# Optimization experiments

Measured on AMD Instinct MI355X. Metric: run time of the kernel, lower is better.

## Reference

```python
import jax, jax.numpy as jnp
import numpy as np

N_BOX = 1000000


def box2corners(box):
    # box: (N,5) = x,y,w,h,alpha -> corners (N,4,2), order matches lilanxiao/Rotated_IoU
    x, y, w, h, a = (box[:, i] for i in range(5))
    dx = jnp.array([0.5, -0.5, -0.5, 0.5], box.dtype)
    dy = jnp.array([0.5, 0.5, -0.5, -0.5], box.dtype)
    cx = dx[None, :] * w[:, None]
    cy = dy[None, :] * h[:, None]
    c, s = jnp.cos(a)[:, None], jnp.sin(a)[:, None]
    rx = cx * c - cy * s + x[:, None]
    ry = cx * s + cy * c + y[:, None]
    return jnp.stack([rx, ry], axis=-1)


def edge_intersections(c1, c2):
    # all 4x4 edge-pair intersections; strict interior criterion (0<t<1, 0<u<1)
    p1, p2 = c1, jnp.roll(c1, -1, axis=1)
    p3, p4 = c2, jnp.roll(c2, -1, axis=1)
    x1, y1 = p1[:, :, None, 0], p1[:, :, None, 1]
    x2, y2 = p2[:, :, None, 0], p2[:, :, None, 1]
    x3, y3 = p3[:, None, :, 0], p3[:, None, :, 1]
    x4, y4 = p4[:, None, :, 0], p4[:, None, :, 1]
    num_t = (x2 - x1) * (y3 - y1) - (y2 - y1) * (x3 - x1)
    den_t = (x2 - x1) * (y3 - y4) - (y2 - y1) * (x3 - x4)
    t = jnp.where(den_t == 0., -1., num_t / jnp.where(den_t == 0., 1., den_t))
    mask_t = (t > 0.) & (t < 1.)
    num_u = (x4 - x3) * (y1 - y3) - (y4 - y3) * (x1 - x3)
    den_u = (x4 - x3) * (y1 - y2) - (y4 - y3) * (x1 - x2)
    u = jnp.where(den_u == 0., -1., num_u / jnp.where(den_u == 0., 1., den_u))
    mask = mask_t & (u > 0.) & (u < 1.)
    tx = x1 + t * (x2 - x1)
    ty = y1 + t * (y2 - y1)
    pts = jnp.stack([tx, ty], axis=-1) * mask[..., None]
    n = c1.shape[0]
    return pts.reshape(n, 16, 2), mask.reshape(n, 16)


def box_in_box(corners1, corners2):
    # projection test: is each corner of box1 inside rectangle box2
    a = corners2[:, 0:1, :]
    b = corners2[:, 1:2, :]
    d = corners2[:, 3:4, :]
    ab, ad, am = b - a, d - a, corners1 - a
    p_ab = (ab * am).sum(-1) / (ab * ab).sum(-1)
    p_ad = (ad * am).sum(-1) / (ad * ad).sum(-1)
    eps = 1e-6
    return (p_ab > -eps) & (p_ab < 1. + eps) & (p_ad > -eps) & (p_ad < 1. + eps)


def intersection_area(c1, c2):
    # convex intersection polygon: 24 candidate vertices, sort valid ones by angle, shoelace
    pts, m_int = edge_intersections(c1, c2)
    m1 = box_in_box(c1, c2)
    m2 = box_in_box(c2, c1)
    verts = jnp.concatenate([c1, c2, pts], axis=1)   # (N,24,2)
    mask = jnp.concatenate([m1, m2, m_int], axis=1)  # (N,24)
    k = mask.sum(axis=1)
    mean = (verts * mask[..., None]).sum(1, keepdims=True) / jnp.maximum(k, 1)[:, None, None]
    v = jnp.where(mask[..., None], verts - mean, 0.)
    ang = jnp.where(mask, jnp.arctan2(v[..., 1], v[..., 0]), 1e9)
    order = jnp.argsort(ang, axis=1)
    vs = jnp.take_along_axis(v, order[..., None], axis=1)
    pad = jnp.arange(24)[None, :, None] < k[:, None, None]
    vs = jnp.where(pad, vs, vs[:, 0:1, :])  # pad by repeating first valid vertex -> zero cross terms
    vn = jnp.roll(vs, -1, axis=1)
    cross = vs[..., 0] * vn[..., 1] - vs[..., 1] * vn[..., 0]
    return 0.5 * jnp.abs(cross.sum(axis=1))


def riou_loss(pred, target):
    # RIOUloss(reduction='none', loss_type='iou') -> cal_diou per-box loss, loss[0]
    rad_p = jnp.arctan2(pred[:, 4], pred[:, 5])
    rad_t = jnp.arctan2(target[:, 4], target[:, 5])
    b1 = jnp.concatenate([pred[:, :4], rad_p[:, None]], axis=1)
    b2 = jnp.concatenate([target[:, :4], rad_t[:, None]], axis=1)
    c1 = box2corners(b1)
    c2 = box2corners(b2)
    inter = intersection_area(c1, c2)
    area1 = b1[:, 2] * b1[:, 3]
    area2 = b2[:, 2] * b2[:, 3]
    union = area1 + area2 - inter
    iou = inter / union
    allc = jnp.concatenate([c1, c2], axis=1)  # (N,8,2) enclosing box (axis-aligned)
    wc = allc[..., 0].max(1) - allc[..., 0].min(1)
    hc = allc[..., 1].max(1) - allc[..., 1].min(1)
    c2diag = wc * wc + hc * hc
    d2 = (b1[:, 0] - b2[:, 0]) ** 2 + (b1[:, 1] - b2[:, 1]) ** 2
    return 1. - iou + d2 / c2diag


def setup_inputs() -> dict:
    key = jax.random.key(0)
    k1, k2, k3, k4 = jax.random.split(key, 4)
    n = N_BOX
    xy = jax.random.uniform(k1, (n, 2)) * 640.
    wh = jax.random.uniform(k2, (n, 2)) * 48. + 2.
    sc = jax.random.normal(k3, (n, 2)) + 0.1
    pred = jnp.concatenate([xy, wh, sc], axis=1)
    k5, k6, k7 = jax.random.split(k4, 3)
    t_xy = xy + jax.random.normal(k5, (n, 2)) * 8.
    t_wh = jnp.abs(wh * (1. + 0.2 * jax.random.normal(k6, (n, 2)))) + 1.
    t_sc = sc + 0.3 * jax.random.normal(k7, (n, 2))
    target = jnp.concatenate([t_xy, t_wh, t_sc], axis=1)
    return {"pred": pred, "target": target}


def reference(pred, target):
    return riou_loss(pred, target)
```

## Files before the change

kernel.cpp:

```cpp
#include <hip/hip_runtime.h>
#include <math.h>


#define FMUL __fmul_rn
#define FADD __fadd_rn
#define FSUB __fsub_rn
#define FDIV __fdiv_rn

__device__ __forceinline__ float rcpf_(float x) { return __builtin_amdgcn_rcpf(x); }

#define CE(A,B) do { unsigned _x = pk[A], _y = pk[B]; \
                     pk[A] = _x < _y ? _x : _y; pk[B] = _x < _y ? _y : _x; } while (0)

#define SORT8(o) do { \
    CE(o+0,o+1); CE(o+2,o+3); CE(o+0,o+2); CE(o+1,o+3); CE(o+1,o+2); \
    CE(o+4,o+5); CE(o+6,o+7); CE(o+4,o+6); CE(o+5,o+7); CE(o+5,o+6); \
    CE(o+0,o+4); CE(o+1,o+5); CE(o+2,o+6); CE(o+3,o+7); \
    CE(o+2,o+4); CE(o+3,o+5); \
    CE(o+1,o+2); CE(o+3,o+4); CE(o+5,o+6); } while (0)

#define MERGE_LOW8(o) do { \
    CE(0,o+7); CE(1,o+6); CE(2,o+5); CE(3,o+4); \
    CE(4,o+3); CE(5,o+2); CE(6,o+1); CE(7,o+0); \
    CE(0,4); CE(1,5); CE(2,6); CE(3,7); \
    CE(0,2); CE(1,3); CE(4,6); CE(5,7); \
    CE(0,1); CE(2,3); CE(4,5); CE(6,7); } while (0)

#define MAKEKEY(J, WX, WY, M, DST) do {                                     \
    float _dsum = FADD(fabsf(WX), fabsf(WY));                               \
    float _rs = (_dsum > 0.0f) ? FMUL((WX), rcpf_(_dsum)) : 1.0f;           \
    float _keyf = copysignf(FSUB(1.0f, _rs), (WY));                         \
    unsigned _sbk = __float_as_uint(_keyf);                                 \
    unsigned _u = _sbk ^ (unsigned)(((int)_sbk >> 31) | (int)0x80000000);   \
    (DST) = (M) ? ((_u & 0xFFFFFFE0u) | (unsigned)(J))                      \
                : (0xFFFFFFE0u | (unsigned)(J));                            \
} while (0)

__global__
__attribute__((amdgpu_flat_work_group_size(256, 256), amdgpu_waves_per_eu(1)))
void riou_kernel(const float* __restrict__ pred,
                 const float* __restrict__ tgt,
                 float* __restrict__ out, int n)
{
    __shared__ float2 vlds[24][256];
    const int tid = threadIdx.x;
    int i = blockIdx.x * blockDim.x + tid;
    if (i >= n) return;

    const float2* p2 = (const float2*)(pred + 6 * (size_t)i);
    const float2* q2 = (const float2*)(tgt  + 6 * (size_t)i);
    float2 pa = p2[0], pb = p2[1], pc2 = p2[2];
    float2 qa = q2[0], qb = q2[1], qc2 = q2[2];
    const float px = pa.x, py = pa.y, pw = pb.x, ph = pb.y;
    const float qx = qa.x, qy = qa.y, qw = qb.x, qh = qb.y;

    float rad1 = atan2f(pc2.x, pc2.y);
    float cA = cosf(rad1), sA = sinf(rad1);
    float rad2 = atan2f(qc2.x, qc2.y);
    float cB = cosf(rad2), sB = sinf(rad2);

    const float ddx[4] = {0.5f, -0.5f, -0.5f, 0.5f};
    const float ddy[4] = {0.5f, 0.5f, -0.5f, -0.5f};
    float c1x[4], c1y[4], c2x[4], c2y[4];
#pragma unroll
    for (int j = 0; j < 4; j++) {
        float cx = FMUL(ddx[j], pw), cy = FMUL(ddy[j], ph);
        c1x[j] = FADD(FSUB(FMUL(cx, cA), FMUL(cy, sA)), px);
        c1y[j] = FADD(FADD(FMUL(cx, sA), FMUL(cy, cA)), py);
        float dx2 = FMUL(ddx[j], qw), dy2 = FMUL(ddy[j], qh);
        c2x[j] = FADD(FSUB(FMUL(dx2, cB), FMUL(dy2, sB)), qx);
        c2y[j] = FADD(FADD(FMUL(dx2, sB), FMUL(dy2, cB)), qy);
        vlds[j][tid]     = make_float2(c1x[j], c1y[j]);
        vlds[4 + j][tid] = make_float2(c2x[j], c2y[j]);
    }

    float minx = c1x[0], maxx = c1x[0], miny = c1y[0], maxy = c1y[0];
#pragma unroll
    for (int j = 1; j < 4; j++) {
        minx = fminf(minx, c1x[j]); maxx = fmaxf(maxx, c1x[j]);
        miny = fminf(miny, c1y[j]); maxy = fmaxf(maxy, c1y[j]);
    }
#pragma unroll
    for (int j = 0; j < 4; j++) {
        minx = fminf(minx, c2x[j]); maxx = fmaxf(maxx, c2x[j]);
        miny = fminf(miny, c2y[j]); maxy = fmaxf(maxy, c2y[j]);
    }
    float wcb = FSUB(maxx, minx), hcb = FSUB(maxy, miny);
    float c2d = FADD(FMUL(wcb, wcb), FMUL(hcb, hcb));
    float dxc = FSUB(px, qx), dyc = FSUB(py, qy);
    float d2 = FADD(FMUL(dxc, dxc), FMUL(dyc, dyc));

    unsigned mbits = 0;
    float sx = 0.0f, sy = 0.0f;
    const float eps = 1e-6f;
    const float hieps = 1.0f + 1e-6f;

    {
        float ax = c2x[0], ay = c2y[0];
        float abx = FSUB(c2x[1], ax), aby = FSUB(c2y[1], ay);
        float adx = FSUB(c2x[3], ax), ady = FSUB(c2y[3], ay);
        float rab = rcpf_(FADD(FMUL(abx, abx), FMUL(aby, aby)));
        float rad = rcpf_(FADD(FMUL(adx, adx), FMUL(ady, ady)));
#pragma unroll
        for (int j = 0; j < 4; j++) {
            float amx = FSUB(c1x[j], ax), amy = FSUB(c1y[j], ay);
            float pab = FMUL(FADD(FMUL(abx, amx), FMUL(aby, amy)), rab);
            float pad = FMUL(FADD(FMUL(adx, amx), FMUL(ady, amy)), rad);
            int m = (pab > -eps) & (pab < hieps) & (pad > -eps) & (pad < hieps);
            mbits |= (unsigned)m << j;
            sx = FADD(sx, m ? c1x[j] : 0.0f);
            sy = FADD(sy, m ? c1y[j] : 0.0f);
        }
    }
    {
        float ax = c1x[0], ay = c1y[0];
        float abx = FSUB(c1x[1], ax), aby = FSUB(c1y[1], ay);
        float adx = FSUB(c1x[3], ax), ady = FSUB(c1y[3], ay);
        float rab = rcpf_(FADD(FMUL(abx, abx), FMUL(aby, aby)));
        float rad = rcpf_(FADD(FMUL(adx, adx), FMUL(ady, ady)));
#pragma unroll
        for (int j = 0; j < 4; j++) {
            float amx = FSUB(c2x[j], ax), amy = FSUB(c2y[j], ay);
            float pab = FMUL(FADD(FMUL(abx, amx), FMUL(aby, amy)), rab);
            float pad = FMUL(FADD(FMUL(adx, amx), FMUL(ady, amy)), rad);
            int m = (pab > -eps) & (pab < hieps) & (pad > -eps) & (pad < hieps);
            mbits |= (unsigned)m << (4 + j);
            sx = FADD(sx, m ? c2x[j] : 0.0f);
            sy = FADD(sy, m ? c2y[j] : 0.0f);
        }
    }
    float fex[4], fey[4];
#pragma unroll
    for (int e2 = 0; e2 < 4; e2++) {
        fex[e2] = FSUB(c2x[(e2 + 1) & 3], c2x[e2]);
        fey[e2] = FSUB(c2y[(e2 + 1) & 3], c2y[e2]);
    }
#pragma unroll
    for (int e1 = 0; e1 < 4; e1++) {
        float x1 = c1x[e1], y1 = c1y[e1];
        float ex = FSUB(c1x[(e1 + 1) & 3], x1), ey = FSUB(c1y[(e1 + 1) & 3], y1);
#pragma unroll
        for (int e2 = 0; e2 < 4; e2++) {
            float dx31 = FSUB(c2x[e2], x1), dy31 = FSUB(c2y[e2], y1);
            float num_t = FSUB(FMUL(ex, dy31), FMUL(ey, dx31));
            float den_t = FSUB(FMUL(ey, fex[e2]), FMUL(ex, fey[e2]));
            float rd = rcpf_(den_t);
            float tq = FMUL(num_t, rd);
            float num_u = FSUB(FMUL(fey[e2], dx31), FMUL(fex[e2], dy31));
            float uq = FMUL(num_u, rd);
            int m = (tq > 0.0f) & (tq < 1.0f) & (uq < 0.0f) & (uq > -1.0f);
            float ix = FADD(x1, FMUL(tq, ex));
            float iy = FADD(y1, FMUL(tq, ey));
            int s = 4 * e1 + e2;
            vlds[8 + s][tid] = make_float2(ix, iy);
            mbits |= (unsigned)m << (8 + s);
            sx = FADD(sx, m ? ix : 0.0f);
            sy = FADD(sy, m ? iy : 0.0f);
        }
    }

    int k = __popc(mbits);

    float kk = (float)(k > 0 ? k : 1);
    float mx = FDIV(sx, kk), my = FDIV(sy, kk);

    unsigned pk[24];
    float2 va[8];
#pragma unroll
    for (int j = 0; j < 8; j++) va[j] = vlds[8 + j][tid];
#pragma unroll
    for (int j = 0; j < 8; j++) {
        float rx = (j < 4) ? c1x[j] : c2x[j - 4];
        float ry = (j < 4) ? c1y[j] : c2y[j - 4];
        int m = (mbits >> j) & 1u;
        float wx2 = FSUB(rx, mx);
        float wy2 = FSUB(ry, my);
        MAKEKEY(j, wx2, wy2, m, pk[j]);
    }
#pragma unroll
    for (int j = 8; j < 16; j++) {
        int m = (mbits >> j) & 1u;
        float wx2 = FSUB(va[j - 8].x, mx);
        float wy2 = FSUB(va[j - 8].y, my);
        MAKEKEY(j, wx2, wy2, m, pk[j]);
    }
#pragma unroll
    for (int j = 0; j < 8; j++) va[j] = vlds[16 + j][tid];
#pragma unroll
    for (int j = 16; j < 24; j++) {
        int m = (mbits >> j) & 1u;
        float wx2 = FSUB(va[j - 16].x, mx);
        float wy2 = FSUB(va[j - 16].y, my);
        MAKEKEY(j, wx2, wy2, m, pk[j]);
    }

    SORT8(0);
    SORT8(8);
    SORT8(16);
    MERGE_LOW8(8);
    MERGE_LOW8(16);

    float2 vi[8];
#pragma unroll
    for (int s = 0; s < 8; s++) {
        unsigned row = pk[s] & 31u;
        vi[s] = vlds[row][tid];
    }

    float firstx = 0.0f, firsty = 0.0f, prevx = 0.0f, prevy = 0.0f;
    float crs = 0.0f;
#pragma unroll
    for (int s = 0; s < 8; s++) {
        float gx = FSUB(vi[s].x, mx);
        float gy = FSUB(vi[s].y, my);
        bool act = s < k;
        float bx = act ? gx : prevx;
        float by = act ? gy : prevy;
        if (s == 0) { firstx = bx; firsty = by; }
        else {
            crs = FADD(crs, FSUB(FMUL(prevx, by), FMUL(prevy, bx)));
        }
        prevx = bx; prevy = by;
    }
    if (k > 8) {
        for (int s = 8; s < k; s++) {
            unsigned mn = pk[8];
#pragma unroll
            for (int j = 9; j < 24; j++) mn = (pk[j] < mn) ? pk[j] : mn;
            float2 vt = vlds[mn & 31u][tid];
            float bx = FSUB(vt.x, mx);
            float by = FSUB(vt.y, my);
            crs = FADD(crs, FSUB(FMUL(prevx, by), FMUL(prevy, bx)));
            prevx = bx; prevy = by;
#pragma unroll
            for (int j = 8; j < 24; j++) if (pk[j] == mn) pk[j] = 0xFFFFFFFFu;
        }
    }
    crs = FADD(crs, FSUB(FMUL(prevx, firsty), FMUL(prevy, firstx)));
    float inter = FMUL(0.5f, fabsf(crs));

    float area1 = FMUL(pw, ph), area2 = FMUL(qw, qh);
    float uni = FSUB(FADD(area1, area2), inter);
    float iou = FMUL(inter, rcpf_(uni));

    out[i] = FADD(FSUB(1.0f, iou), FMUL(d2, rcpf_(c2d)));
}

extern "C" void kernel_launch(void* const* d_in, const int* in_sizes, int n_in,
                              void* d_out, int out_size, void* d_ws, size_t ws_size,
                              hipStream_t stream) {
    const float* pred = (const float*)d_in[0];
    const float* tgt  = (const float*)d_in[1];
    float* out = (float*)d_out;
    int n = in_sizes[0] / 6;
    int block = 256;
    int grid = (n + block - 1) / block;
    riou_kernel<<<grid, block, 0, stream>>>(pred, tgt, out, n);
}
```

Measured before the change: 110.5 us.

## Vectorize geometry with packed float2 math and split LDS into SoA rows

```diff
diff --git a/kernel.cpp b/kernel.cpp
--- a/kernel.cpp
+++ b/kernel.cpp
@@ -7,6 +7,9 @@
 #define FSUB __fsub_rn
 #define FDIV __fdiv_rn
 
+typedef float v2f __attribute__((ext_vector_type(2)));
+__device__ __forceinline__ v2f v2(float a, float b) { v2f r; r.x = a; r.y = b; return r; }
+__device__ __forceinline__ v2f vs(float a) { return v2(a, a); }
 __device__ __forceinline__ float rcpf_(float x) { return __builtin_amdgcn_rcpf(x); }
 
 #define CE(A,B) do { unsigned _x = pk[A], _y = pk[B]; \
@@ -36,13 +39,16 @@
                 : (0xFFFFFFE0u | (unsigned)(J));                            \
 } while (0)
 
+#define LN(P, J) (((J) & 1) ? P[(J) >> 1].y : P[(J) >> 1].x)
+
 __global__
 __attribute__((amdgpu_flat_work_group_size(256, 256), amdgpu_waves_per_eu(1)))
 void riou_kernel(const float* __restrict__ pred,
                  const float* __restrict__ tgt,
                  float* __restrict__ out, int n)
 {
-    __shared__ float2 vlds[24][256];
+    __shared__ __align__(16) float ldsX[256][26];
+    __shared__ __align__(16) float ldsY[256][26];
     const int tid = threadIdx.x;
     int i = blockIdx.x * blockDim.x + tid;
     if (i >= n) return;
@@ -54,36 +60,47 @@
     const float px = pa.x, py = pa.y, pw = pb.x, ph = pb.y;
     const float qx = qa.x, qy = qa.y, qw = qb.x, qh = qb.y;
 
+    float area1 = FMUL(pw, ph), area2 = FMUL(qw, qh);
+
     float rad1 = atan2f(pc2.x, pc2.y);
     float cA = cosf(rad1), sA = sinf(rad1);
     float rad2 = atan2f(qc2.x, qc2.y);
     float cB = cosf(rad2), sB = sinf(rad2);
 
-    const float ddx[4] = {0.5f, -0.5f, -0.5f, 0.5f};
-    const float ddy[4] = {0.5f, 0.5f, -0.5f, -0.5f};
-    float c1x[4], c1y[4], c2x[4], c2y[4];
+    v2f c1xp[2], c1yp[2], c2xp[2], c2yp[2];
+    {
+        const v2f dx01 = v2(0.5f, -0.5f), dx23 = v2(-0.5f, 0.5f);
+        const v2f dy01 = v2(0.5f, 0.5f),  dy23 = v2(-0.5f, -0.5f);
+        v2f cxx01 = dx01 * vs(pw), cxx23 = dx23 * vs(pw);
+        v2f cyy01 = dy01 * vs(ph), cyy23 = dy23 * vs(ph);
+        c1xp[0] = (cxx01 * vs(cA) - cyy01 * vs(sA)) + vs(px);
+        c1xp[1] = (cxx23 * vs(cA) - cyy23 * vs(sA)) + vs(px);
+        c1yp[0] = (cxx01 * vs(sA) + cyy01 * vs(cA)) + vs(py);
+        c1yp[1] = (cxx23 * vs(sA) + cyy23 * vs(cA)) + vs(py);
+        v2f qxx01 = dx01 * vs(qw), qxx23 = dx23 * vs(qw);
+        v2f qyy01 = dy01 * vs(qh), qyy23 = dy23 * vs(qh);
+        c2xp[0] = (qxx01 * vs(cB) - qyy01 * vs(sB)) + vs(qx);
+        c2xp[1] = (qxx23 * vs(cB) - qyy23 * vs(sB)) + vs(qx);
+        c2yp[0] = (qxx01 * vs(sB) + qyy01 * vs(cB)) + vs(qy);
+        c2yp[1] = (qxx23 * vs(sB) + qyy23 * vs(cB)) + vs(qy);
+    }
+    *(v2f*)&ldsX[tid][0] = c1xp[0]; *(v2f*)&ldsX[tid][2] = c1xp[1];
+    *(v2f*)&ldsX[tid][4] = c2xp[0]; *(v2f*)&ldsX[tid][6] = c2xp[1];
+    *(v2f*)&ldsY[tid][0] = c1yp[0]; *(v2f*)&ldsY[tid][2] = c1yp[1];
+    *(v2f*)&ldsY[tid][4] = c2yp[0]; *(v2f*)&ldsY[tid][6] = c2yp[1];
+
+    float minx = c1xp[0].x, maxx = c1xp[0].x;
+    float miny = c1yp[0].x, maxy = c1yp[0].x;
+    minx = fminf(minx, c1xp[0].y); maxx = fmaxf(maxx, c1xp[0].y);
+    miny = fminf(miny, c1yp[0].y); maxy = fmaxf(maxy, c1yp[0].y);
+    minx = fminf(minx, c1xp[1].x); maxx = fmaxf(maxx, c1xp[1].x);
+    miny = fminf(miny, c1yp[1].x); maxy = fmaxf(maxy, c1yp[1].x);
+    minx = fminf(minx, c1xp[1].y); maxx = fmaxf(maxx, c1xp[1].y);
+    miny = fminf(miny, c1yp[1].y); maxy = fmaxf(maxy, c1yp[1].y);
 #pragma unroll
     for (int j = 0; j < 4; j++) {
-        float cx = FMUL(ddx[j], pw), cy = FMUL(ddy[j], ph);
-        c1x[j] = FADD(FSUB(FMUL(cx, cA), FMUL(cy, sA)), px);
-        c1y[j] = FADD(FADD(FMUL(cx, sA), FMUL(cy, cA)), py);
-        float dx2 = FMUL(ddx[j], qw), dy2 = FMUL(ddy[j], qh);
-        c2x[j] = FADD(FSUB(FMUL(dx2, cB), FMUL(dy2, sB)), qx);
-        c2y[j] = FADD(FADD(FMUL(dx2, sB), FMUL(dy2, cB)), qy);
-        vlds[j][tid]     = make_float2(c1x[j], c1y[j]);
-        vlds[4 + j][tid] = make_float2(c2x[j], c2y[j]);
-    }
-
-    float minx = c1x[0], maxx = c1x[0], miny = c1y[0], maxy = c1y[0];
-#pragma unroll
-    for (int j = 1; j < 4; j++) {
-        minx = fminf(minx, c1x[j]); maxx = fmaxf(maxx, c1x[j]);
-        miny = fminf(miny, c1y[j]); maxy = fmaxf(maxy, c1y[j]);
-    }
-#pragma unroll
-    for (int j = 0; j < 4; j++) {
-        minx = fminf(minx, c2x[j]); maxx = fmaxf(maxx, c2x[j]);
-        miny = fminf(miny, c2y[j]); maxy = fmaxf(maxy, c2y[j]);
+        minx = fminf(minx, LN(c2xp, j)); maxx = fmaxf(maxx, LN(c2xp, j));
+        miny = fminf(miny, LN(c2yp, j)); maxy = fmaxf(maxy, LN(c2yp, j));
     }
     float wcb = FSUB(maxx, minx), hcb = FSUB(maxy, miny);
     float c2d = FADD(FMUL(wcb, wcb), FMUL(hcb, hcb));
@@ -91,128 +108,187 @@
     float d2 = FADD(FMUL(dxc, dxc), FMUL(dyc, dyc));
 
     unsigned mbits = 0;
-    float sx = 0.0f, sy = 0.0f;
+    v2f s2 = v2(0.0f, 0.0f);
+    const v2f zero2 = v2(0.0f, 0.0f);
     const float eps = 1e-6f;
     const float hieps = 1.0f + 1e-6f;
 
     {
-        float ax = c2x[0], ay = c2y[0];
-        float abx = FSUB(c2x[1], ax), aby = FSUB(c2y[1], ay);
-        float adx = FSUB(c2x[3], ax), ady = FSUB(c2y[3], ay);
+        float ax = c2xp[0].x, ay = c2yp[0].x;
+        float abx = FSUB(c2xp[0].y, ax), aby = FSUB(c2yp[0].y, ay);
+        float adx = FSUB(c2xp[1].y, ax), ady = FSUB(c2yp[1].y, ay);
         float rab = rcpf_(FADD(FMUL(abx, abx), FMUL(aby, aby)));
         float rad = rcpf_(FADD(FMUL(adx, adx), FMUL(ady, ady)));
+        v2f amx01 = c1xp[0] - vs(ax), amx23 = c1xp[1] - vs(ax);
+        v2f amy01 = c1yp[0] - vs(ay), amy23 = c1yp[1] - vs(ay);
+        v2f pab01 = (vs(abx) * amx01 + vs(aby) * amy01) * vs(rab);
+        v2f pab23 = (vs(abx) * amx23 + vs(aby) * amy23) * vs(rab);
+        v2f pad01 = (vs(adx) * amx01 + vs(ady) * amy01) * vs(rad);
+        v2f pad23 = (vs(adx) * amx23 + vs(ady) * amy23) * vs(rad);
 #pragma unroll
         for (int j = 0; j < 4; j++) {
-            float amx = FSUB(c1x[j], ax), amy = FSUB(c1y[j], ay);
-            float pab = FMUL(FADD(FMUL(abx, amx), FMUL(aby, amy)), rab);
-            float pad = FMUL(FADD(FMUL(adx, amx), FMUL(ady, amy)), rad);
+            float pab = (j < 2) ? ((j & 1) ? pab01.y : pab01.x)
+                                : ((j & 1) ? pab23.y : pab23.x);
+            float pad = (j < 2) ? ((j & 1) ? pad01.y : pad01.x)
+                                : ((j & 1) ? pad23.y : pad23.x);
             int m = (pab > -eps) & (pab < hieps) & (pad > -eps) & (pad < hieps);
             mbits |= (unsigned)m << j;
-            sx = FADD(sx, m ? c1x[j] : 0.0f);
-            sy = FADD(sy, m ? c1y[j] : 0.0f);
-        }
-    }
-    {
-        float ax = c1x[0], ay = c1y[0];
-        float abx = FSUB(c1x[1], ax), aby = FSUB(c1y[1], ay);
-        float adx = FSUB(c1x[3], ax), ady = FSUB(c1y[3], ay);
+            s2 = s2 + (m ? v2(LN(c1xp, j), LN(c1yp, j)) : zero2);
+        }
+    }
+    {
+        float ax = c1xp[0].x, ay = c1yp[0].x;
+        float abx = FSUB(c1xp[0].y, ax), aby = FSUB(c1yp[0].y, ay);
+        float adx = FSUB(c1xp[1].y, ax), ady = FSUB(c1yp[1].y, ay);
         float rab = rcpf_(FADD(FMUL(abx, abx), FMUL(aby, aby)));
         float rad = rcpf_(FADD(FMUL(adx, adx), FMUL(ady, ady)));
+        v2f amx01 = c2xp[0] - vs(ax), amx23 = c2xp[1] - vs(ax);
+        v2f amy01 = c2yp[0] - vs(ay), amy23 = c2yp[1] - vs(ay);
+        v2f pab01 = (vs(abx) * amx01 + vs(aby) * amy01) * vs(rab);
+        v2f pab23 = (vs(abx) * amx23 + vs(aby) * amy23) * vs(rab);
+        v2f pad01 = (vs(adx) * amx01 + vs(ady) * amy01) * vs(rad);
+        v2f pad23 = (vs(adx) * amx23 + vs(ady) * amy23) * vs(rad);
 #pragma unroll
         for (int j = 0; j < 4; j++) {
-            float amx = FSUB(c2x[j], ax), amy = FSUB(c2y[j], ay);
-            float pab = FMUL(FADD(FMUL(abx, amx), FMUL(aby, amy)), rab);
-            float pad = FMUL(FADD(FMUL(adx, amx), FMUL(ady, amy)), rad);
+            float pab = (j < 2) ? ((j & 1) ? pab01.y : pab01.x)
+                                : ((j & 1) ? pab23.y : pab23.x);
+            float pad = (j < 2) ? ((j & 1) ? pad01.y : pad01.x)
+                                : ((j & 1) ? pad23.y : pad23.x);
             int m = (pab > -eps) & (pab < hieps) & (pad > -eps) & (pad < hieps);
             mbits |= (unsigned)m << (4 + j);
-            sx = FADD(sx, m ? c2x[j] : 0.0f);
-            sy = FADD(sy, m ? c2y[j] : 0.0f);
-        }
-    }
-    float fex[4], fey[4];
-#pragma unroll
-    for (int e2 = 0; e2 < 4; e2++) {
-        fex[e2] = FSUB(c2x[(e2 + 1) & 3], c2x[e2]);
-        fey[e2] = FSUB(c2y[(e2 + 1) & 3], c2y[e2]);
-    }
+            s2 = s2 + (m ? v2(LN(c2xp, j), LN(c2yp, j)) : zero2);
+        }
+    }
+    v2f fexx01, fexx23, feyy01, feyy23;
+    fexx01.x = FSUB(c2xp[0].y, c2xp[0].x);
+    fexx01.y = FSUB(c2xp[1].x, c2xp[0].y);
+    fexx23.x = FSUB(c2xp[1].y, c2xp[1].x);
+    fexx23.y = FSUB(c2xp[0].x, c2xp[1].y);
+    feyy01.x = FSUB(c2yp[0].y, c2yp[0].x);
+    feyy01.y = FSUB(c2yp[1].x, c2yp[0].y);
+    feyy23.x = FSUB(c2yp[1].y, c2yp[1].x);
+    feyy23.y = FSUB(c2yp[0].x, c2yp[1].y);
 #pragma unroll
     for (int e1 = 0; e1 < 4; e1++) {
-        float x1 = c1x[e1], y1 = c1y[e1];
-        float ex = FSUB(c1x[(e1 + 1) & 3], x1), ey = FSUB(c1y[(e1 + 1) & 3], y1);
+        float x1 = LN(c1xp, e1), y1 = LN(c1yp, e1);
+        float xn = LN(c1xp, (e1 + 1) & 3), yn = LN(c1yp, (e1 + 1) & 3);
+        float ex = FSUB(xn, x1), ey = FSUB(yn, y1);
+        v2f d31x01 = c2xp[0] - vs(x1), d31x23 = c2xp[1] - vs(x1);
+        v2f d31y01 = c2yp[0] - vs(y1), d31y23 = c2yp[1] - vs(y1);
+        v2f numt01 = vs(ex) * d31y01 - vs(ey) * d31x01;
+        v2f numt23 = vs(ex) * d31y23 - vs(ey) * d31x23;
+        v2f dent01 = vs(ey) * fexx01 - vs(ex) * feyy01;
+        v2f dent23 = vs(ey) * fexx23 - vs(ex) * feyy23;
+        v2f rd01, rd23;
+        rd01.x = rcpf_(dent01.x); rd01.y = rcpf_(dent01.y);
+        rd23.x = rcpf_(dent23.x); rd23.y = rcpf_(dent23.y);
+        v2f tq01 = numt01 * rd01, tq23 = numt23 * rd23;
+        v2f numu01 = feyy01 * d31x01 - fexx01 * d31y01;
+        v2f numu23 = feyy23 * d31x23 - fexx23 * d31y23;
+        v2f uq01 = numu01 * rd01, uq23 = numu23 * rd23;
+        v2f ixx01 = vs(x1) + tq01 * vs(ex), ixx23 = vs(x1) + tq23 * vs(ex);
+        v2f iyy01 = vs(y1) + tq01 * vs(ey), iyy23 = vs(y1) + tq23 * vs(ey);
+        int cb = 8 + 4 * e1;
+        *(v2f*)&ldsX[tid][cb]     = ixx01;
+        *(v2f*)&ldsX[tid][cb + 2] = ixx23;
+        *(v2f*)&ldsY[tid][cb]     = iyy01;
+        *(v2f*)&ldsY[tid][cb + 2] = iyy23;
 #pragma unroll
         for (int e2 = 0; e2 < 4; e2++) {
-            float dx31 = FSUB(c2x[e2], x1), dy31 = FSUB(c2y[e2], y1);
-            float num_t = FSUB(FMUL(ex, dy31), FMUL(ey, dx31));
-            float den_t = FSUB(FMUL(ey, fex[e2]), FMUL(ex, fey[e2]));
-            float rd = rcpf_(den_t);
-            float tq = FMUL(num_t, rd);
-            float num_u = FSUB(FMUL(fey[e2], dx31), FMUL(fex[e2], dy31));
-            float uq = FMUL(num_u, rd);
+            float tq = (e2 < 2) ? ((e2 & 1) ? tq01.y : tq01.x)
+                                : ((e2 & 1) ? tq23.y : tq23.x);
+            float uq = (e2 < 2) ? ((e2 & 1) ? uq01.y : uq01.x)
+                                : ((e2 & 1) ? uq23.y : uq23.x);
+            float ixv = (e2 < 2) ? ((e2 & 1) ? ixx01.y : ixx01.x)
+                                 : ((e2 & 1) ? ixx23.y : ixx23.x);
+            float iyv = (e2 < 2) ? ((e2 & 1) ? iyy01.y : iyy01.x)
+                                 : ((e2 & 1) ? iyy23.y : iyy23.x);
             int m = (tq > 0.0f) & (tq < 1.0f) & (uq < 0.0f) & (uq > -1.0f);
-            float ix = FADD(x1, FMUL(tq, ex));
-            float iy = FADD(y1, FMUL(tq, ey));
-            int s = 4 * e1 + e2;
-            vlds[8 + s][tid] = make_float2(ix, iy);
-            mbits |= (unsigned)m << (8 + s);
-            sx = FADD(sx, m ? ix : 0.0f);
-            sy = FADD(sy, m ? iy : 0.0f);
+            mbits |= (unsigned)m << (cb + e2);
+            s2 = s2 + (m ? v2(ixv, iyv) : zero2);
         }
     }
 
     int k = __popc(mbits);
 
     float kk = (float)(k > 0 ? k : 1);
-    float mx = FDIV(sx, kk), my = FDIV(sy, kk);
+    float mx = FDIV(s2.x, kk), my = FDIV(s2.y, kk);
 
     unsigned pk[24];
-    float2 va[8];
-#pragma unroll
-    for (int j = 0; j < 8; j++) va[j] = vlds[8 + j][tid];
-#pragma unroll
-    for (int j = 0; j < 8; j++) {
-        float rx = (j < 4) ? c1x[j] : c2x[j - 4];
-        float ry = (j < 4) ? c1y[j] : c2y[j - 4];
-        int m = (mbits >> j) & 1u;
-        float wx2 = FSUB(rx, mx);
-        float wy2 = FSUB(ry, my);
-        MAKEKEY(j, wx2, wy2, m, pk[j]);
-    }
-#pragma unroll
-    for (int j = 8; j < 16; j++) {
-        int m = (mbits >> j) & 1u;
-        float wx2 = FSUB(va[j - 8].x, mx);
-        float wy2 = FSUB(va[j - 8].y, my);
-        MAKEKEY(j, wx2, wy2, m, pk[j]);
-    }
-#pragma unroll
-    for (int j = 0; j < 8; j++) va[j] = vlds[16 + j][tid];
-#pragma unroll
-    for (int j = 16; j < 24; j++) {
-        int m = (mbits >> j) & 1u;
-        float wx2 = FSUB(va[j - 16].x, mx);
-        float wy2 = FSUB(va[j - 16].y, my);
-        MAKEKEY(j, wx2, wy2, m, pk[j]);
-    }
-
+    v2f bx0 = *(v2f*)&ldsX[tid][8],  bx1 = *(v2f*)&ldsX[tid][10];
+    v2f bx2 = *(v2f*)&ldsX[tid][12], bx3 = *(v2f*)&ldsX[tid][14];
+    v2f by0 = *(v2f*)&ldsY[tid][8],  by1 = *(v2f*)&ldsY[tid][10];
+    v2f by2 = *(v2f*)&ldsY[tid][12], by3 = *(v2f*)&ldsY[tid][14];
+    {
+        v2f wx, wy;
+        wx = c1xp[0] - vs(mx); wy = c1yp[0] - vs(my);
+        MAKEKEY(0, wx.x, wy.x, (int)((mbits >> 0) & 1u), pk[0]);
+        MAKEKEY(1, wx.y, wy.y, (int)((mbits >> 1) & 1u), pk[1]);
+        wx = c1xp[1] - vs(mx); wy = c1yp[1] - vs(my);
+        MAKEKEY(2, wx.x, wy.x, (int)((mbits >> 2) & 1u), pk[2]);
+        MAKEKEY(3, wx.y, wy.y, (int)((mbits >> 3) & 1u), pk[3]);
+        wx = c2xp[0] - vs(mx); wy = c2yp[0] - vs(my);
+        MAKEKEY(4, wx.x, wy.x, (int)((mbits >> 4) & 1u), pk[4]);
+        MAKEKEY(5, wx.y, wy.y, (int)((mbits >> 5) & 1u), pk[5]);
+        wx = c2xp[1] - vs(mx); wy = c2yp[1] - vs(my);
+        MAKEKEY(6, wx.x, wy.x, (int)((mbits >> 6) & 1u), pk[6]);
+        MAKEKEY(7, wx.y, wy.y, (int)((mbits >> 7) & 1u), pk[7]);
+    }
     SORT8(0);
+    {
+        v2f wx, wy;
+        wx = bx0 - vs(mx); wy = by0 - vs(my);
+        MAKEKEY(8, wx.x, wy.x, (int)((mbits >> 8) & 1u), pk[8]);
+        MAKEKEY(9, wx.y, wy.y, (int)((mbits >> 9) & 1u), pk[9]);
+        wx = bx1 - vs(mx); wy = by1 - vs(my);
+        MAKEKEY(10, wx.x, wy.x, (int)((mbits >> 10) & 1u), pk[10]);
+        MAKEKEY(11, wx.y, wy.y, (int)((mbits >> 11) & 1u), pk[11]);
+        wx = bx2 - vs(mx); wy = by2 - vs(my);
+        MAKEKEY(12, wx.x, wy.x, (int)((mbits >> 12) & 1u), pk[12]);
+        MAKEKEY(13, wx.y, wy.y, (int)((mbits >> 13) & 1u), pk[13]);
+        wx = bx3 - vs(mx); wy = by3 - vs(my);
+        MAKEKEY(14, wx.x, wy.x, (int)((mbits >> 14) & 1u), pk[14]);
+        MAKEKEY(15, wx.y, wy.y, (int)((mbits >> 15) & 1u), pk[15]);
+    }
+    bx0 = *(v2f*)&ldsX[tid][16]; bx1 = *(v2f*)&ldsX[tid][18];
+    bx2 = *(v2f*)&ldsX[tid][20]; bx3 = *(v2f*)&ldsX[tid][22];
+    by0 = *(v2f*)&ldsY[tid][16]; by1 = *(v2f*)&ldsY[tid][18];
+    by2 = *(v2f*)&ldsY[tid][20]; by3 = *(v2f*)&ldsY[tid][22];
     SORT8(8);
+    {
+        v2f wx, wy;
+        wx = bx0 - vs(mx); wy = by0 - vs(my);
+        MAKEKEY(16, wx.x, wy.x, (int)((mbits >> 16) & 1u), pk[16]);
+        MAKEKEY(17, wx.y, wy.y, (int)((mbits >> 17) & 1u), pk[17]);
+        wx = bx1 - vs(mx); wy = by1 - vs(my);
+        MAKEKEY(18, wx.x, wy.x, (int)((mbits >> 18) & 1u), pk[18]);
+        MAKEKEY(19, wx.y, wy.y, (int)((mbits >> 19) & 1u), pk[19]);
+        wx = bx2 - vs(mx); wy = by2 - vs(my);
+        MAKEKEY(20, wx.x, wy.x, (int)((mbits >> 20) & 1u), pk[20]);
+        MAKEKEY(21, wx.y, wy.y, (int)((mbits >> 21) & 1u), pk[21]);
+        wx = bx3 - vs(mx); wy = by3 - vs(my);
+        MAKEKEY(22, wx.x, wy.x, (int)((mbits >> 22) & 1u), pk[22]);
+        MAKEKEY(23, wx.y, wy.y, (int)((mbits >> 23) & 1u), pk[23]);
+    }
+
     SORT8(16);
     MERGE_LOW8(8);
     MERGE_LOW8(16);
 
-    float2 vi[8];
+    float gxv[8], gyv[8];
 #pragma unroll
     for (int s = 0; s < 8; s++) {
         unsigned row = pk[s] & 31u;
-        vi[s] = vlds[row][tid];
+        gxv[s] = ldsX[tid][row];
+        gyv[s] = ldsY[tid][row];
     }
 
     float firstx = 0.0f, firsty = 0.0f, prevx = 0.0f, prevy = 0.0f;
     float crs = 0.0f;
 #pragma unroll
     for (int s = 0; s < 8; s++) {
-        float gx = FSUB(vi[s].x, mx);
-        float gy = FSUB(vi[s].y, my);
+        float gx = FSUB(gxv[s], mx);
+        float gy = FSUB(gyv[s], my);
         bool act = s < k;
         float bx = act ? gx : prevx;
         float by = act ? gy : prevy;
@@ -227,9 +303,9 @@
             unsigned mn = pk[8];
 #pragma unroll
             for (int j = 9; j < 24; j++) mn = (pk[j] < mn) ? pk[j] : mn;
-            float2 vt = vlds[mn & 31u][tid];
-            float bx = FSUB(vt.x, mx);
-            float by = FSUB(vt.y, my);
+            unsigned row = mn & 31u;
+            float bx = FSUB(ldsX[tid][row], mx);
+            float by = FSUB(ldsY[tid][row], my);
             crs = FADD(crs, FSUB(FMUL(prevx, by), FMUL(prevy, bx)));
             prevx = bx; prevy = by;
 #pragma unroll
@@ -239,7 +315,6 @@
     crs = FADD(crs, FSUB(FMUL(prevx, firsty), FMUL(prevy, firstx)));
     float inter = FMUL(0.5f, fabsf(crs));
 
-    float area1 = FMUL(pw, ph), area2 = FMUL(qw, qh);
     float uni = FSUB(FADD(area1, area2), inter);
     float iou = FMUL(inter, rcpf_(uni));
 
```

Measured after the change: 111.5 us. No clear change (+0.9%).
